# Optimization experiments

Hardware: AMD Instinct MI355X
Metric: run time of the kernel (lower is better)

## Reference

```python
import jax, jax.numpy as jnp
import numpy as np

# Locally-connected 2D convolution (torch legacy SpatialConvolutionLocal)
# out[b,o,h,w] = sum_{c,i,j} weight[h,w,o,c,i,j] * x_pad[b,c,h*dH+i,w*dW+j] + bias[o,h,w]

B, CIN, IH, IW = 32, 32, 64, 64
COUT, KH, KW = 64, 3, 3
DH, DW = 1, 1
PADH, PADW = 1, 1
OH = (IH + 2 * PADH - KH) // DH + 1
OW = (IW + 2 * PADW - KW) // DW + 1


def setup_inputs() -> dict:
    key = jax.random.key(0)
    k1, k2, k3 = jax.random.split(key, 3)
    stdv = 1.0 / np.sqrt(KW * KH * CIN)
    x = jax.random.normal(k1, (B, CIN, IH, IW), dtype=jnp.float32)
    weight = jax.random.uniform(k2, (OH, OW, COUT, CIN, KH, KW), dtype=jnp.float32,
                                minval=-stdv, maxval=stdv)
    bias = jax.random.uniform(k3, (COUT, OH, OW), dtype=jnp.float32,
                              minval=-stdv, maxval=stdv)
    return {"x": x, "weight": weight, "bias": bias}


def _extract_patches(x):
    # x: [B, C, IH, IW] -> patches [B, C, KH, KW, OH, OW]
    xp = jnp.pad(x, ((0, 0), (0, 0), (PADH, PADH), (PADW, PADW)))
    rows = []
    for i in range(KH):  # small fixed kernel loop (9 iters), not a data-dim loop
        cols = []
        for j in range(KW):
            cols.append(xp[:, :, i:i + OH * DH:DH, j:j + OW * DW:DW])
        rows.append(jnp.stack(cols, axis=2))  # [B, C, KW, OH, OW]
    return jnp.stack(rows, axis=2)  # [B, C, KH, KW, OH, OW]


def reference(x, weight, bias):
    patches = _extract_patches(x)  # [B, C, KH, KW, OH, OW]
    # per-position GEMM: distinct weight matrix at each (h, w)
    out = jnp.einsum('bcijhw,hwocij->bohw', patches, weight)
    return out + bias[None]  # [B, COUT, OH, OW]
```

## Files before the change

kernel.cpp:

```cpp
#include <hip/hip_runtime.h>


typedef __attribute__((ext_vector_type(8))) short short8;
typedef __attribute__((ext_vector_type(16))) float f32x16;
typedef __attribute__((ext_vector_type(4))) float f32x4;

__device__ __forceinline__ unsigned f2bf(float f) {
    unsigned u = __builtin_bit_cast(unsigned, f);
    return (u + 0x7FFFu + ((u >> 16) & 1u)) >> 16;
}

__device__ __forceinline__ void glds16(const float* g, float* l) {
    __builtin_amdgcn_global_load_lds(
        (const __attribute__((address_space(1))) void*)g,
        (__attribute__((address_space(3))) void*)l, 16, 0, 0);
}

__global__ __launch_bounds__(256, 1) void lcconv_kernel(
    const float* __restrict__ xg,
    const float* __restrict__ wg,
    const float* __restrict__ bg,
    float* __restrict__ outg)
{
    __shared__ __align__(16) unsigned char Lds[147456];
    float*          Wring = (float*)Lds;
    unsigned short* Xl    = (unsigned short*)(Lds + 73728);
    float*          Pred  = (float*)(Lds + 110592);
    float*          outF  = (float*)(Lds + 114688);
    (void)Wring;

    const int tid = threadIdx.x;
    const int Bq  = blockIdx.x;
    const int xcd = Bq & 7;
    const int idx = Bq >> 3;
    const int h   = xcd * 8 + (idx >> 4);
    const int w0  = (idx & 15) * 4;

    const int lane = tid & 63;
    const int wv   = tid >> 6;
    const int n    = lane & 31;
    const int g    = lane >> 5;
    const int oh   = wv >> 1;
    const int kh   = wv & 1;

    int srcoff[9];
#pragma unroll
    for (int j = 0; j < 9; j++) {
        int P  = wv * 576 + j * 64 + lane;
        int rp = (P * 3641) >> 18;
        int qp = P - rp * 72;
        srcoff[j] = rp * 1152 + ((qp ^ (rp & 7)) << 4);
    }

    {
        const char* rb = (const char*)(wg + ((h * 64 + w0) * 64) * 288);
        float* db = (float*)(Lds + wv * 9216);
#pragma unroll
        for (int j = 0; j < 9; j++)
            glds16((const float*)(rb + srcoff[j]), db + j * 256);
    }

#pragma unroll
    for (int t = 0; t < 12; t++) {
        int task = t * 256 + tid;
        int b   = task / 96;
        int rem = task - b * 96;
        int c   = rem / 3;
        int y3  = rem - c * 3;
        int y   = h + y3 - 1;
        float v0 = 0.f, v1 = 0.f, v2 = 0.f, v3 = 0.f, v4 = 0.f, v5 = 0.f;
        if ((unsigned)y < 64u) {
            const float* row = xg + ((b * 32 + c) * 64 + y) * 64;
            float4 m = *(const float4*)(row + w0);
            v1 = m.x; v2 = m.y; v3 = m.z; v4 = m.w;
            if (w0 > 0)      v0 = row[w0 - 1];
            if (w0 + 4 < 64) v5 = row[w0 + 4];
        }
        int cr = (c + b) & 31;
        unsigned* dst = (unsigned*)(Xl + ((b * 32 + cr) * 3 + y3) * 6);
        dst[0] = f2bf(v0) | (f2bf(v1) << 16);
        dst[1] = f2bf(v2) | (f2bf(v3) << 16);
        dst[2] = f2bf(v4) | (f2bf(v5) << 16);
    }
    __syncthreads();

    f32x16 acc;
#pragma unroll
    for (int i = 0; i < 16; i++) acc[i] = 0.f;

    const int kh144  = kh * 144, kh36 = kh * 36;
    const int g8     = g * 8,    g2   = g * 2;
    const int nn1152 = n * 1152, n7   = n & 7;

    for (int ph = 0; ph < 8; ph++) {
        __syncthreads();

        if (ph < 7) {
            int p1 = ph + 1;
            const char* rb = (const char*)(
                wg + ((h * 64 + w0 + (p1 >> 1)) * 64 + (p1 & 1) * 32) * 288);
            float* db = (float*)(Lds + (p1 & 1) * 36864 + wv * 9216);
#pragma unroll
            for (int j = 0; j < 9; j++)
                glds16((const float*)(rb + srcoff[j]), db + j * 256);
        }

        const int active = (oh == (ph & 1));
        const int pos    = ph >> 1;
        if (active) {
            const char* Wt = (const char*)Lds + (ph & 1) * 36864;
            const int   ab = n * 576 + pos;
#pragma unroll
            for (int s = 0; s < 9; s++) {
                int q0 = kh36 + s * 4 + g2;
                f32x4 wa = *(const f32x4*)(Wt + nn1152 + (((q0    ) ^ n7) << 4));
                f32x4 wb = *(const f32x4*)(Wt + nn1152 + (((q0 + 1) ^ n7) << 4));

                short8 a;
#pragma unroll
                for (int e = 0; e < 8; e++) {
                    int k  = kh144 + s * 16 + g8 + e;
                    int c  = (k * 456) >> 12;
                    int t2 = k - c * 9;
                    int i  = (t2 * 11) >> 5;
                    int j2 = t2 - i * 3;
                    int cr = (c + n) & 31;
                    a[e] = (short)Xl[ab + cr * 18 + i * 6 + j2];
                }

                short8 w8;
                w8[0] = (short)f2bf(wa[0]); w8[1] = (short)f2bf(wa[1]);
                w8[2] = (short)f2bf(wa[2]); w8[3] = (short)f2bf(wa[3]);
                w8[4] = (short)f2bf(wb[0]); w8[5] = (short)f2bf(wb[1]);
                w8[6] = (short)f2bf(wb[2]); w8[7] = (short)f2bf(wb[3]);

                acc = __builtin_amdgcn_mfma_f32_32x32x16_bf16(a, w8, acc, 0, 0, 0);
            }
            if (kh == 0) {
#pragma unroll
                for (int r = 0; r < 16; r++) Pred[r * 64 + lane] = acc[r];
            }
        }
        __syncthreads();

        if (active && kh == 1) {
#pragma unroll
            for (int r = 0; r < 16; r++) {
                float v = acc[r] + Pred[r * 64 + lane];
                int b = (r & 3) + 8 * (r >> 2) + 4 * g;
                outF[((oh * 4 + pos) * 32 + b) * 32 + n] = v;
            }
        }
        if (active) {
#pragma unroll
            for (int i2 = 0; i2 < 16; i2++) acc[i2] = 0.f;
        }
    }
    __syncthreads();

#pragma unroll
    for (int it = 0; it < 8; it++) {
        int id = it * 256 + tid;
        int b  = id >> 6;
        int o  = id & 63;
        const float* src = outF + (o >> 5) * 4096 + b * 32 + (o & 31);
        float4 v;
        v.x = src[0];
        v.y = src[1024];
        v.z = src[2048];
        v.w = src[3072];
        const float4 bb = *(const float4*)(bg + (o * 64 + h) * 64 + w0);
        v.x += bb.x; v.y += bb.y; v.z += bb.z; v.w += bb.w;
        *(float4*)(outg + ((b * 64 + o) * 64 + h) * 64 + w0) = v;
    }
}

extern "C" void kernel_launch(void* const* d_in, const int* in_sizes, int n_in,
                              void* d_out, int out_size, void* d_ws, size_t ws_size,
                              hipStream_t stream) {
    const float* x = (const float*)d_in[0];
    const float* w = (const float*)d_in[1];
    const float* b = (const float*)d_in[2];
    float* out = (float*)d_out;
    lcconv_kernel<<<dim3(1024), dim3(256), 0, stream>>>(x, w, b, out);
}
```

Baseline: 469.9 us.

## Triple-buffer weight loads with vmcnt waits and defer k-split reduction to end

Weight tiles now go through a three-slot LDS ring with a prefetch distance of two phases. A counted s_waitcnt vmcnt plus a raw s_barrier replaces the two __syncthreads per phase. Each wave keeps four accumulator sets, one per output position, so the per-phase Pred exchange and the second barrier are gone; the kh halves are combined once at the end through LDS. This aims to hide global-load latency and cut barrier stalls, at the cost of 48 more accumulator VGPRs and a correctness dependence on the hand-written waitcnt counts and barrier placement.

```diff
diff --git a/kernel.cpp b/kernel.cpp
--- a/kernel.cpp
+++ b/kernel.cpp
@@ -23,11 +23,7 @@
     float* __restrict__ outg)
 {
     __shared__ __align__(16) unsigned char Lds[147456];
-    float*          Wring = (float*)Lds;
-    unsigned short* Xl    = (unsigned short*)(Lds + 73728);
-    float*          Pred  = (float*)(Lds + 110592);
-    float*          outF  = (float*)(Lds + 114688);
-    (void)Wring;
+    unsigned short* Xl = (unsigned short*)(Lds + 110592);
 
     const int tid = threadIdx.x;
     const int Bq  = blockIdx.x;
@@ -52,9 +48,12 @@
         srcoff[j] = rp * 1152 + ((qp ^ (rp & 7)) << 4);
     }
 
-    {
-        const char* rb = (const char*)(wg + ((h * 64 + w0) * 64) * 288);
-        float* db = (float*)(Lds + wv * 9216);
+    const char* wtile = (const char*)(wg + (h * 64 + w0) * 64 * 288);
+
+#pragma unroll
+    for (int ph = 0; ph < 2; ph++) {
+        const char* rb = wtile + (ph >> 1) * 73728 + (ph & 1) * 36864;
+        float* db = (float*)(Lds + (ph % 3) * 36864 + wv * 9216);
 #pragma unroll
         for (int j = 0; j < 9; j++)
             glds16((const float*)(rb + srcoff[j]), db + j * 256);
@@ -84,32 +83,38 @@
     }
     __syncthreads();
 
-    f32x16 acc;
+    f32x16 accP[4];
 #pragma unroll
-    for (int i = 0; i < 16; i++) acc[i] = 0.f;
+    for (int p = 0; p < 4; p++)
+#pragma unroll
+        for (int i = 0; i < 16; i++) accP[p][i] = 0.f;
 
     const int kh144  = kh * 144, kh36 = kh * 36;
     const int g8     = g * 8,    g2   = g * 2;
     const int nn1152 = n * 1152, n7   = n & 7;
+    const int ab0    = n * 576;
 
+#pragma unroll
     for (int ph = 0; ph < 8; ph++) {
-        __syncthreads();
+        if (ph < 7) asm volatile("s_waitcnt vmcnt(9)" ::: "memory");
+        else        asm volatile("s_waitcnt vmcnt(0)" ::: "memory");
+        __builtin_amdgcn_sched_barrier(0);
+        __builtin_amdgcn_s_barrier();
+        __builtin_amdgcn_sched_barrier(0);
 
-        if (ph < 7) {
-            int p1 = ph + 1;
-            const char* rb = (const char*)(
-                wg + ((h * 64 + w0 + (p1 >> 1)) * 64 + (p1 & 1) * 32) * 288);
-            float* db = (float*)(Lds + (p1 & 1) * 36864 + wv * 9216);
+        if (ph + 2 < 8) {
+            const char* rb = wtile + ((ph + 2) >> 1) * 73728
+                                   + ((ph + 2) & 1) * 36864;
+            float* db = (float*)(Lds + ((ph + 2) % 3) * 36864 + wv * 9216);
 #pragma unroll
             for (int j = 0; j < 9; j++)
                 glds16((const float*)(rb + srcoff[j]), db + j * 256);
         }
 
-        const int active = (oh == (ph & 1));
-        const int pos    = ph >> 1;
-        if (active) {
-            const char* Wt = (const char*)Lds + (ph & 1) * 36864;
-            const int   ab = n * 576 + pos;
+        if (oh == (ph & 1)) {
+            const char* Wt  = (const char*)Lds + (ph % 3) * 36864;
+            const int   pos = ph >> 1;
+            const int   ab  = ab0 + pos;
 #pragma unroll
             for (int s = 0; s < 9; s++) {
                 int q0 = kh36 + s * 4 + g2;
@@ -134,27 +139,31 @@
                 w8[4] = (short)f2bf(wb[0]); w8[5] = (short)f2bf(wb[1]);
                 w8[6] = (short)f2bf(wb[2]); w8[7] = (short)f2bf(wb[3]);
 
-                acc = __builtin_amdgcn_mfma_f32_32x32x16_bf16(a, w8, acc, 0, 0, 0);
-            }
-            if (kh == 0) {
-#pragma unroll
-                for (int r = 0; r < 16; r++) Pred[r * 64 + lane] = acc[r];
+                accP[pos] = __builtin_amdgcn_mfma_f32_32x32x16_bf16(
+                    a, w8, accP[pos], 0, 0, 0);
             }
         }
-        __syncthreads();
+    }
 
-        if (active && kh == 1) {
+    float* outF = (float*)Lds;
+    if (kh == 0) {
+#pragma unroll
+        for (int pos = 0; pos < 4; pos++)
 #pragma unroll
             for (int r = 0; r < 16; r++) {
-                float v = acc[r] + Pred[r * 64 + lane];
                 int b = (r & 3) + 8 * (r >> 2) + 4 * g;
-                outF[((oh * 4 + pos) * 32 + b) * 32 + n] = v;
+                outF[((oh * 4 + pos) * 32 + b) * 32 + n] = accP[pos][r];
             }
-        }
-        if (active) {
+    }
+    __syncthreads();
+    if (kh == 1) {
 #pragma unroll
-            for (int i2 = 0; i2 < 16; i2++) acc[i2] = 0.f;
-        }
+        for (int pos = 0; pos < 4; pos++)
+#pragma unroll
+            for (int r = 0; r < 16; r++) {
+                int b = (r & 3) + 8 * (r >> 2) + 4 * g;
+                outF[((oh * 4 + pos) * 32 + b) * 32 + n] += accP[pos][r];
+            }
     }
     __syncthreads();
 
```

Result: slower. 523.4 us (+11.4%).
